# Performance work log

Measured on AMD Instinct MI355X. Metric: run time of the kernel, lower is better.

## Reference

```python
import jax, jax.numpy as jnp
import numpy as np

B, S, H = 2, 2048, 2048          # batch, seq, hidden_size
E, K = 16, 4                     # n_routed_experts, num_experts_per_tok
I = 1408                         # moe_intermediate_size
NS = 2                           # n_shared_experts
SI = I * NS                      # shared-expert intermediate size


def _mlp(x, wg, wu, wd):
    # SwiGLU MLP: down( silu(gate(x)) * up(x) )
    return (jax.nn.silu(x @ wg.T) * (x @ wu.T)) @ wd.T


def setup_inputs() -> dict:
    key = jax.random.key(0)
    ks = jax.random.split(key, 8)
    sc = lambda k, shape, fan: (jax.random.normal(k, shape, jnp.float32) * (fan ** -0.5))
    return {
        "hidden_states": jax.random.normal(ks[0], (B, S, H), jnp.float32),
        "gate_w": sc(ks[1], (E, H), H),          # router logits weight
        "w_gate": sc(ks[2], (E, I, H), H),       # per-expert gate_proj
        "w_up": sc(ks[3], (E, I, H), H),         # per-expert up_proj
        "w_down": sc(ks[4], (E, H, I), I),       # per-expert down_proj
        "sw_gate": sc(ks[5], (SI, H), H),        # shared-expert gate_proj
        "sw_up": sc(ks[6], (SI, H), H),
        "sw_down": sc(ks[7], (H, SI), SI),
    }


def reference(hidden_states, gate_w, w_gate, w_up, w_down, sw_gate, sw_up, sw_down):
    x = hidden_states.reshape(-1, H)                     # [T, H]
    T = x.shape[0]
    # --- MoEGate: softmax scoring, top-k, normalize weights to sum 1 ---
    scores = jax.nn.softmax(x @ gate_w.T, axis=-1)       # [T, E]
    topk_w, topk_idx = jax.lax.top_k(scores, K)          # [T, K]
    topk_w = topk_w / jnp.sum(topk_w, axis=-1, keepdims=True)
    # Dense combine weights [T, E]: cw[t, e] = sum_k 1[topk_idx==e] * topk_w
    cw = jnp.zeros((T, E), x.dtype).at[jnp.arange(T)[:, None], topk_idx].add(topk_w)
    # --- dispatch / per-expert MLP / weighted combine (scan over experts) ---
    def step(acc, p):
        wg, wu, wd, w = p                                # w: [T] combine weight
        return acc + w[:, None] * _mlp(x, wg, wu, wd), None
    y, _ = jax.lax.scan(step, jnp.zeros_like(x), (w_gate, w_up, w_down, cw.T))
    y = y.reshape(hidden_states.shape)
    # --- shared experts ---
    return y + _mlp(hidden_states, sw_gate, sw_up, sw_down)
```

## Files before the change

kernel.cpp:

```cpp
#include <hip/hip_runtime.h>
#include <cstdint>
#include <cstddef>

#define TTOK 4096
#define HID  2048
#define NEXP 16
#define KTOP 4
#define IMID 1408
#define SIM  2816

typedef __attribute__((ext_vector_type(4))) float f32x4;
typedef __attribute__((ext_vector_type(8))) short s16x8;
typedef __attribute__((ext_vector_type(4))) short s16x4;

#define OFF_XB   0UL
#define OFF_WGB  (OFF_XB  + 16777216UL)
#define OFF_WUB  (OFF_WGB + 92274688UL)
#define OFF_WDB  (OFF_WUB + 92274688UL)
#define OFF_SWG  (OFF_WDB + 92274688UL)
#define OFF_SWU  (OFF_SWG + 11534336UL)
#define OFF_SWD  (OFF_SWU + 11534336UL)
#define OFF_TKI  (OFF_SWD + 11534336UL)
#define OFF_TKW  (OFF_TKI + 65536UL)
#define OFF_CNT  (OFF_TKW + 65536UL)
#define OFF_OFFS (OFF_CNT + 64UL)
#define OFF_CUR  (OFF_OFFS + 64UL)
#define OFF_LIST (OFF_CUR + 64UL)
#define OFF_ACT  (OFF_LIST + 65536UL)
#define OFF_DOUT (OFF_ACT + 46137344UL)
#define OFF_SACT OFF_ACT

__device__ __forceinline__ unsigned short f2bf(float f) {
    unsigned int u = __float_as_uint(f);
    return (unsigned short)((u + 0x7FFFu + ((u >> 16) & 1u)) >> 16);
}
__device__ __forceinline__ float bf2f(unsigned short s) {
    return __uint_as_float(((unsigned int)s) << 16);
}
__device__ __forceinline__ void gll16(const void* g, void* l) {
    __builtin_amdgcn_global_load_lds((const __attribute__((address_space(1))) unsigned int*)g,
                                     (__attribute__((address_space(3))) unsigned int*)l, 16, 0, 0);
}

__global__ __launch_bounds__(256) void cast_k(const float* __restrict__ in,
                                              unsigned short* __restrict__ out, long n) {
    long i = ((long)blockIdx.x * 256 + threadIdx.x) * 4;
    if (i >= n) return;
    f32x4 v = *(const f32x4*)(in + i);
    s16x4 o;
    o.x = (short)f2bf(v.x); o.y = (short)f2bf(v.y);
    o.z = (short)f2bf(v.z); o.w = (short)f2bf(v.w);
    *(s16x4*)(out + i) = o;
}

__global__ __launch_bounds__(64) void route_k(const float* __restrict__ x,
                                              const float* __restrict__ gw,
                                              int* __restrict__ tki, float* __restrict__ tkw) {
    int t = blockIdx.x;
    int lane = threadIdx.x;
    const float* xr = x + (size_t)t * HID;
    float acc[NEXP];
#pragma unroll
    for (int e = 0; e < NEXP; e++) acc[e] = 0.f;
    for (int h = lane; h < HID; h += 64) {
        float xv = xr[h];
#pragma unroll
        for (int e = 0; e < NEXP; e++) acc[e] += xv * gw[e * HID + h];
    }
#pragma unroll
    for (int e = 0; e < NEXP; e++) {
        float v = acc[e];
#pragma unroll
        for (int off = 32; off; off >>= 1) v += __shfl_xor(v, off);
        acc[e] = v;
    }
    if (lane == 0) {
        float mx = acc[0];
#pragma unroll
        for (int e = 1; e < NEXP; e++) mx = fmaxf(mx, acc[e]);
        float s = 0.f, p[NEXP];
#pragma unroll
        for (int e = 0; e < NEXP; e++) { p[e] = expf(acc[e] - mx); s += p[e]; }
#pragma unroll
        for (int e = 0; e < NEXP; e++) p[e] /= s;
        float wsum = 0.f; int idx[KTOP]; float wv[KTOP];
#pragma unroll
        for (int k = 0; k < KTOP; k++) {
            int bi = 0; float bv = -1.f;
#pragma unroll
            for (int e = 0; e < NEXP; e++) if (p[e] > bv) { bv = p[e]; bi = e; }
            idx[k] = bi; wv[k] = bv; p[bi] = -2.f; wsum += bv;
        }
#pragma unroll
        for (int k = 0; k < KTOP; k++) { tki[t * 4 + k] = idx[k]; tkw[t * 4 + k] = wv[k] / wsum; }
    }
}

__global__ __launch_bounds__(256) void count_k(const int* __restrict__ tki, int* __restrict__ cnt) {
    int i = blockIdx.x * 256 + threadIdx.x;
    if (i < TTOK * KTOP) atomicAdd(&cnt[tki[i]], 1);
}
__global__ void scan_k(const int* __restrict__ cnt, int* __restrict__ offs, int* __restrict__ cur) {
    if (threadIdx.x == 0) {
        int s = 0;
        for (int e = 0; e < NEXP; e++) { offs[e] = s; cur[e] = s; s += cnt[e]; }
    }
}
__global__ __launch_bounds__(256) void scatter_k(const int* __restrict__ tki, int* __restrict__ cur,
                                                 int* __restrict__ list) {
    int i = blockIdx.x * 256 + threadIdx.x;
    if (i < TTOK * KTOP) {
        int e = tki[i];
        int p = atomicAdd(&cur[e], 1);
        list[p] = i;
    }
}

template <int MODE>
__global__ __launch_bounds__(256, 2) void gemm_k(const unsigned short* __restrict__ A,
                                                 const unsigned short* __restrict__ B0,
                                                 const unsigned short* __restrict__ B1,
                                                 void* __restrict__ C,
                                                 const int* __restrict__ counts,
                                                 const int* __restrict__ offs,
                                                 const int* __restrict__ list,
                                                 const float* __restrict__ tkw) {
    constexpr bool GU = (MODE == 0 || MODE == 1);
    constexpr bool ROUTED = (MODE == 0 || MODE == 2);
    constexpr int KD = (MODE == 2) ? IMID : ((MODE == 3) ? SIM : HID);
    constexpr int ND = (MODE == 0) ? IMID : ((MODE == 1) ? SIM : HID);
    constexpr int NB = ND / 128;

    int tid = threadIdx.x, lane = tid & 63, wv = tid >> 6;
    int bid = blockIdx.x;
    int e = 0, mb, nb, cnt, off;
    if (ROUTED) {
        e = bid / (32 * NB);
        int r = bid - e * (32 * NB);
        mb = r / NB; nb = r - mb * NB;
        cnt = counts[e]; off = offs[e];
        if (mb * 128 >= cnt) return;
    } else {
        mb = bid / NB; nb = bid - mb * NB; cnt = TTOK; off = 0;
    }

    const unsigned short* b0 = B0;
    const unsigned short* b1 = B1;
    if (MODE == 0) { b0 += (size_t)e * IMID * HID; b1 += (size_t)e * IMID * HID; }
    if (MODE == 2) { b0 += (size_t)e * HID * IMID; }

    const char* arow[2];
    const char* brow0[2];
    const char* brow1[2];
#pragma unroll
    for (int q = 0; q < 2; q++) {
        int r = mb * 128 + q * 64 + (tid >> 2);
        int rr = r < cnt ? r : cnt - 1;
        if (MODE == 0) { int tk = list[off + rr] >> 2; arow[q] = (const char*)(A + (size_t)tk * HID); }
        if (MODE == 1) { arow[q] = (const char*)(A + (size_t)rr * HID); }
        if (MODE == 2) { arow[q] = (const char*)(A + (size_t)(off + rr) * IMID); }
        if (MODE == 3) { arow[q] = (const char*)(A + (size_t)rr * SIM); }
        int rn = nb * 128 + q * 64 + (tid >> 2);
        brow0[q] = (const char*)(b0 + (size_t)rn * KD);
        if (GU) brow1[q] = (const char*)(b1 + (size_t)rn * KD);
    }

    constexpr int SBYTES = GU ? 24576 : 16384;
    __shared__ __align__(64) char smem[SBYTES];
    int inner = (lane & 3) * 16;
    char* ldsA  = smem + wv * 1024;
    char* ldsB0 = smem + 8192 + wv * 1024;
    char* ldsB1 = smem + 16384 + wv * 1024;

    f32x4 acc0[4][4], acc1[4][4];
#pragma unroll
    for (int i = 0; i < 4; i++)
#pragma unroll
        for (int j = 0; j < 4; j++) {
            acc0[i][j] = (f32x4){0.f, 0.f, 0.f, 0.f};
            acc1[i][j] = (f32x4){0.f, 0.f, 0.f, 0.f};
        }

    int wm = wv >> 1, wn = wv & 1;
    const unsigned short* rA  = (const unsigned short*)smem +
                                (wm * 64 + (lane & 15)) * 32 + ((lane >> 4) << 3);
    const unsigned short* rB0 = (const unsigned short*)(smem + 8192) +
                                (wn * 64 + (lane & 15)) * 32 + ((lane >> 4) << 3);
    const unsigned short* rB1 = (const unsigned short*)(smem + 16384) +
                                (wn * 64 + (lane & 15)) * 32 + ((lane >> 4) << 3);

    for (int k0 = 0; k0 < KD; k0 += 32) {
        size_t kb = (size_t)k0 * 2 + inner;
#pragma unroll
        for (int q = 0; q < 2; q++) {
            gll16(arow[q] + kb, ldsA + q * 4096);
            gll16(brow0[q] + kb, ldsB0 + q * 4096);
            if (GU) gll16(brow1[q] + kb, ldsB1 + q * 4096);
        }
        asm volatile("s_waitcnt vmcnt(0)" ::: "memory");
        __syncthreads();

        s16x8 af[4], bf0[4], bf1[4];
#pragma unroll
        for (int i = 0; i < 4; i++) {
            af[i] = *(const s16x8*)(rA + i * 16 * 32);
            bf0[i] = *(const s16x8*)(rB0 + i * 16 * 32);
            if (GU) bf1[i] = *(const s16x8*)(rB1 + i * 16 * 32);
        }
#pragma unroll
        for (int mi = 0; mi < 4; mi++)
#pragma unroll
            for (int ni = 0; ni < 4; ni++) {
                acc0[mi][ni] = __builtin_amdgcn_mfma_f32_16x16x32_bf16(af[mi], bf0[ni], acc0[mi][ni], 0, 0, 0);
                if (GU)
                    acc1[mi][ni] = __builtin_amdgcn_mfma_f32_16x16x32_bf16(af[mi], bf1[ni], acc1[mi][ni], 0, 0, 0);
            }
        __syncthreads();
    }

    int c0 = nb * 128 + wn * 64 + (lane & 15);
    int rb = mb * 128 + wm * 64 + ((lane >> 4) << 2);

    if (GU) {
        unsigned short* outp = (unsigned short*)C;
#pragma unroll
        for (int mi = 0; mi < 4; mi++)
#pragma unroll
            for (int j = 0; j < 4; j++) {
                int gr = rb + mi * 16 + j;
                if (gr < cnt) {
                    size_t orow = (size_t)(ROUTED ? (off + gr) : gr);
                    unsigned short* op = outp + orow * ND + c0;
#pragma unroll
                    for (int ni = 0; ni < 4; ni++) {
                        float g = acc0[mi][ni][j], u = acc1[mi][ni][j];
                        float v = (g / (1.f + expf(-g))) * u;
                        op[ni * 16] = f2bf(v);
                    }
                }
            }
    } else if (MODE == 2) {
        unsigned short* outp = (unsigned short*)C;
#pragma unroll
        for (int mi = 0; mi < 4; mi++)
#pragma unroll
            for (int j = 0; j < 4; j++) {
                int gr = rb + mi * 16 + j;
                if (gr < cnt) {
                    int en = list[off + gr];
                    float w = tkw[en];
                    unsigned short* op = outp + (size_t)en * HID + c0;
#pragma unroll
                    for (int ni = 0; ni < 4; ni++) op[ni * 16] = f2bf(acc0[mi][ni][j] * w);
                }
            }
    } else {
        float* outp = (float*)C;
#pragma unroll
        for (int mi = 0; mi < 4; mi++)
#pragma unroll
            for (int j = 0; j < 4; j++) {
                int gr = rb + mi * 16 + j;
                float* op = outp + (size_t)gr * HID + c0;
#pragma unroll
                for (int ni = 0; ni < 4; ni++) op[ni * 16] = acc0[mi][ni][j];
            }
    }
}

__global__ __launch_bounds__(256) void combine_k(const unsigned short* __restrict__ dout,
                                                 float* __restrict__ y) {
    long i = ((long)blockIdx.x * 256 + threadIdx.x) * 4;
    int t = (int)(i >> 11);
    int h = (int)(i & 2047);
    f32x4 acc = *(f32x4*)(y + i);
#pragma unroll
    for (int k = 0; k < 4; k++) {
        s16x4 dv = *(const s16x4*)(dout + (((size_t)t * 4 + k) << 11) + h);
        acc.x += bf2f((unsigned short)dv.x);
        acc.y += bf2f((unsigned short)dv.y);
        acc.z += bf2f((unsigned short)dv.z);
        acc.w += bf2f((unsigned short)dv.w);
    }
    *(f32x4*)(y + i) = acc;
}

extern "C" void kernel_launch(void* const* d_in, const int* in_sizes, int n_in,
                              void* d_out, int out_size, void* d_ws, size_t ws_size,
                              hipStream_t stream) {
    const float* x   = (const float*)d_in[0];
    const float* gw  = (const float*)d_in[1];
    const float* wg  = (const float*)d_in[2];
    const float* wu  = (const float*)d_in[3];
    const float* wd  = (const float*)d_in[4];
    const float* swg = (const float*)d_in[5];
    const float* swu = (const float*)d_in[6];
    const float* swd = (const float*)d_in[7];

    char* ws = (char*)d_ws;
    unsigned short* xb   = (unsigned short*)(ws + OFF_XB);
    unsigned short* wgb  = (unsigned short*)(ws + OFF_WGB);
    unsigned short* wub  = (unsigned short*)(ws + OFF_WUB);
    unsigned short* wdb  = (unsigned short*)(ws + OFF_WDB);
    unsigned short* swgb = (unsigned short*)(ws + OFF_SWG);
    unsigned short* swub = (unsigned short*)(ws + OFF_SWU);
    unsigned short* swdb = (unsigned short*)(ws + OFF_SWD);
    int*   tki  = (int*)(ws + OFF_TKI);
    float* tkw  = (float*)(ws + OFF_TKW);
    int*   cnt  = (int*)(ws + OFF_CNT);
    int*   offs = (int*)(ws + OFF_OFFS);
    int*   cur  = (int*)(ws + OFF_CUR);
    int*   list = (int*)(ws + OFF_LIST);
    unsigned short* act  = (unsigned short*)(ws + OFF_ACT);
    unsigned short* dout = (unsigned short*)(ws + OFF_DOUT);
    unsigned short* sact = (unsigned short*)(ws + OFF_SACT);
    float* y = (float*)d_out;

    hipMemsetAsync(ws + OFF_CNT, 0, 192, stream);

    auto cast = [&](const float* in, unsigned short* out, long n) {
        int blocks = (int)((n / 4 + 255) / 256);
        cast_k<<<blocks, 256, 0, stream>>>(in, out, n);
    };
    cast(x,   xb,   (long)TTOK * HID);
    cast(wg,  wgb,  (long)NEXP * IMID * HID);
    cast(wu,  wub,  (long)NEXP * IMID * HID);
    cast(wd,  wdb,  (long)NEXP * HID * IMID);
    cast(swg, swgb, (long)SIM * HID);
    cast(swu, swub, (long)SIM * HID);
    cast(swd, swdb, (long)HID * SIM);

    route_k<<<TTOK, 64, 0, stream>>>(x, gw, tki, tkw);
    count_k<<<TTOK * KTOP / 256, 256, 0, stream>>>(tki, cnt);
    scan_k<<<1, 64, 0, stream>>>(cnt, offs, cur);
    scatter_k<<<TTOK * KTOP / 256, 256, 0, stream>>>(tki, cur, list);

    gemm_k<0><<<NEXP * 32 * (IMID / 128), 256, 0, stream>>>(xb, wgb, wub, act, cnt, offs, list, tkw);
    gemm_k<2><<<NEXP * 32 * (HID / 128), 256, 0, stream>>>(act, wdb, nullptr, dout, cnt, offs, list, tkw);
    gemm_k<1><<<(TTOK / 128) * (SIM / 128), 256, 0, stream>>>(xb, swgb, swub, sact, cnt, offs, list, tkw);
    gemm_k<3><<<(TTOK / 128) * (HID / 128), 256, 0, stream>>>(sact, swdb, nullptr, (void*)y, cnt, offs, list, tkw);

    combine_k<<<TTOK * HID / 4 / 256, 256, 0, stream>>>(dout, y);
}
```

Baseline: 1.446 ms.

## Double-buffer GEMM LDS staging, swizzle block order, and widen cast vectors

The GEMM main loop now double-buffers LDS, issuing the next K-slice's global-to-LDS loads before computing on the current one. This removes the full wait-then-compute serialization of each iteration. It also adds an MFMA-friendly LDS layout where each lane reads a contiguous 16-byte chunk, a block-index remap that interleaves by 8 and walks M-tiles fastest, s_setprio around the MFMA block, and a launch_bounds occupancy hint of 3. The cast kernel now handles 8 elements per thread. Risks: LDS use doubles, which may limit occupancy, and the remaining vmcnt wait placement is implicit, so prefetched data may not be guaranteed complete before it is read.

```diff
diff --git a/kernel.cpp b/kernel.cpp
--- a/kernel.cpp
+++ b/kernel.cpp
@@ -44,13 +44,16 @@
 
 __global__ __launch_bounds__(256) void cast_k(const float* __restrict__ in,
                                               unsigned short* __restrict__ out, long n) {
-    long i = ((long)blockIdx.x * 256 + threadIdx.x) * 4;
+    long i = ((long)blockIdx.x * 256 + threadIdx.x) * 8;
     if (i >= n) return;
-    f32x4 v = *(const f32x4*)(in + i);
-    s16x4 o;
-    o.x = (short)f2bf(v.x); o.y = (short)f2bf(v.y);
-    o.z = (short)f2bf(v.z); o.w = (short)f2bf(v.w);
-    *(s16x4*)(out + i) = o;
+    f32x4 a = *(const f32x4*)(in + i);
+    f32x4 b = *(const f32x4*)(in + i + 4);
+    s16x8 o;
+    o[0] = (short)f2bf(a.x); o[1] = (short)f2bf(a.y);
+    o[2] = (short)f2bf(a.z); o[3] = (short)f2bf(a.w);
+    o[4] = (short)f2bf(b.x); o[5] = (short)f2bf(b.y);
+    o[6] = (short)f2bf(b.z); o[7] = (short)f2bf(b.w);
+    *(s16x8*)(out + i) = o;
 }
 
 __global__ __launch_bounds__(64) void route_k(const float* __restrict__ x,
@@ -117,7 +120,7 @@
 }
 
 template <int MODE>
-__global__ __launch_bounds__(256, 2) void gemm_k(const unsigned short* __restrict__ A,
+__global__ __launch_bounds__(256, 3) void gemm_k(const unsigned short* __restrict__ A,
                                                  const unsigned short* __restrict__ B0,
                                                  const unsigned short* __restrict__ B1,
                                                  void* __restrict__ C,
@@ -132,16 +135,19 @@
     constexpr int NB = ND / 128;
 
     int tid = threadIdx.x, lane = tid & 63, wv = tid >> 6;
-    int bid = blockIdx.x;
+
+    int nwg8 = (int)gridDim.x >> 3;
+    int bid = (blockIdx.x & 7) * nwg8 + (blockIdx.x >> 3);
+
     int e = 0, mb, nb, cnt, off;
     if (ROUTED) {
         e = bid / (32 * NB);
         int r = bid - e * (32 * NB);
-        mb = r / NB; nb = r - mb * NB;
+        nb = r >> 5; mb = r & 31;
         cnt = counts[e]; off = offs[e];
         if (mb * 128 >= cnt) return;
     } else {
-        mb = bid / NB; nb = bid - mb * NB; cnt = TTOK; off = 0;
+        nb = bid >> 5; mb = bid & 31; cnt = TTOK; off = 0;
     }
 
     const unsigned short* b0 = B0;
@@ -149,28 +155,40 @@
     if (MODE == 0) { b0 += (size_t)e * IMID * HID; b1 += (size_t)e * IMID * HID; }
     if (MODE == 2) { b0 += (size_t)e * HID * IMID; }
 
-    const char* arow[2];
-    const char* brow0[2];
-    const char* brow1[2];
+    const char* asrc[2];
+    const char* b0src[2];
+    const char* b1src[2];
 #pragma unroll
     for (int q = 0; q < 2; q++) {
-        int r = mb * 128 + q * 64 + (tid >> 2);
+        int st = 2 * wv + q;
+        int rt = st * 16 + (lane & 15);
+        int r = mb * 128 + rt;
         int rr = r < cnt ? r : cnt - 1;
-        if (MODE == 0) { int tk = list[off + rr] >> 2; arow[q] = (const char*)(A + (size_t)tk * HID); }
-        if (MODE == 1) { arow[q] = (const char*)(A + (size_t)rr * HID); }
-        if (MODE == 2) { arow[q] = (const char*)(A + (size_t)(off + rr) * IMID); }
-        if (MODE == 3) { arow[q] = (const char*)(A + (size_t)rr * SIM); }
-        int rn = nb * 128 + q * 64 + (tid >> 2);
-        brow0[q] = (const char*)(b0 + (size_t)rn * KD);
-        if (GU) brow1[q] = (const char*)(b1 + (size_t)rn * KD);
-    }
-
-    constexpr int SBYTES = GU ? 24576 : 16384;
-    __shared__ __align__(64) char smem[SBYTES];
-    int inner = (lane & 3) * 16;
-    char* ldsA  = smem + wv * 1024;
-    char* ldsB0 = smem + 8192 + wv * 1024;
-    char* ldsB1 = smem + 16384 + wv * 1024;
+        const unsigned short* ap;
+        if (MODE == 0) { int tk = list[off + rr] >> 2; ap = A + (size_t)tk * HID; }
+        else if (MODE == 1) { ap = A + (size_t)rr * HID; }
+        else if (MODE == 2) { ap = A + (size_t)(off + rr) * IMID; }
+        else { ap = A + (size_t)rr * SIM; }
+        asrc[q] = (const char*)ap + ((lane >> 4) << 4);
+        int rn = nb * 128 + rt;
+        b0src[q] = (const char*)(b0 + (size_t)rn * KD) + ((lane >> 4) << 4);
+        if (GU) b1src[q] = (const char*)(b1 + (size_t)rn * KD) + ((lane >> 4) << 4);
+    }
+
+    constexpr int BUFSZ = GU ? 24576 : 16384;
+    __shared__ __align__(1024) char smem[2 * BUFSZ];
+
+    auto stage = [&](int buf, int k0) {
+        char* base = smem + buf * BUFSZ;
+        size_t kb = (size_t)k0 * 2;
+#pragma unroll
+        for (int q = 0; q < 2; q++) {
+            int st = 2 * wv + q;
+            gll16(asrc[q] + kb, base + st * 1024);
+            gll16(b0src[q] + kb, base + 8192 + st * 1024);
+            if constexpr (GU) gll16(b1src[q] + kb, base + 16384 + st * 1024);
+        }
+    };
 
     f32x4 acc0[4][4], acc1[4][4];
 #pragma unroll
@@ -182,46 +200,44 @@
         }
 
     int wm = wv >> 1, wn = wv & 1;
-    const unsigned short* rA  = (const unsigned short*)smem +
-                                (wm * 64 + (lane & 15)) * 32 + ((lane >> 4) << 3);
-    const unsigned short* rB0 = (const unsigned short*)(smem + 8192) +
-                                (wn * 64 + (lane & 15)) * 32 + ((lane >> 4) << 3);
-    const unsigned short* rB1 = (const unsigned short*)(smem + 16384) +
-                                (wn * 64 + (lane & 15)) * 32 + ((lane >> 4) << 3);
-
+    int raoff = (wm * 4) * 1024 + lane * 16;
+    int rboff = 8192 + (wn * 4) * 1024 + lane * 16;
+    int rb1off = 16384 + (wn * 4) * 1024 + lane * 16;
+
+    stage(0, 0);
+    asm volatile("s_waitcnt vmcnt(0)" ::: "memory");
+    __syncthreads();
+
+    int cur = 0;
     for (int k0 = 0; k0 < KD; k0 += 32) {
-        size_t kb = (size_t)k0 * 2 + inner;
-#pragma unroll
-        for (int q = 0; q < 2; q++) {
-            gll16(arow[q] + kb, ldsA + q * 4096);
-            gll16(brow0[q] + kb, ldsB0 + q * 4096);
-            if (GU) gll16(brow1[q] + kb, ldsB1 + q * 4096);
+        if (k0 + 32 < KD) stage(cur ^ 1, k0 + 32);
+
+        const char* bufp = smem + cur * BUFSZ;
+        s16x8 af[4], bv0[4], bv1[4];
+#pragma unroll
+        for (int i = 0; i < 4; i++) {
+            af[i]  = *(const s16x8*)(bufp + raoff + i * 1024);
+            bv0[i] = *(const s16x8*)(bufp + rboff + i * 1024);
+            if constexpr (GU) bv1[i] = *(const s16x8*)(bufp + rb1off + i * 1024);
         }
-        asm volatile("s_waitcnt vmcnt(0)" ::: "memory");
+        __builtin_amdgcn_s_setprio(1);
+#pragma unroll
+        for (int mi = 0; mi < 4; mi++)
+#pragma unroll
+            for (int ni = 0; ni < 4; ni++) {
+                acc0[mi][ni] = __builtin_amdgcn_mfma_f32_16x16x32_bf16(af[mi], bv0[ni], acc0[mi][ni], 0, 0, 0);
+                if constexpr (GU)
+                    acc1[mi][ni] = __builtin_amdgcn_mfma_f32_16x16x32_bf16(af[mi], bv1[ni], acc1[mi][ni], 0, 0, 0);
+            }
+        __builtin_amdgcn_s_setprio(0);
         __syncthreads();
-
-        s16x8 af[4], bf0[4], bf1[4];
-#pragma unroll
-        for (int i = 0; i < 4; i++) {
-            af[i] = *(const s16x8*)(rA + i * 16 * 32);
-            bf0[i] = *(const s16x8*)(rB0 + i * 16 * 32);
-            if (GU) bf1[i] = *(const s16x8*)(rB1 + i * 16 * 32);
-        }
-#pragma unroll
-        for (int mi = 0; mi < 4; mi++)
-#pragma unroll
-            for (int ni = 0; ni < 4; ni++) {
-                acc0[mi][ni] = __builtin_amdgcn_mfma_f32_16x16x32_bf16(af[mi], bf0[ni], acc0[mi][ni], 0, 0, 0);
-                if (GU)
-                    acc1[mi][ni] = __builtin_amdgcn_mfma_f32_16x16x32_bf16(af[mi], bf1[ni], acc1[mi][ni], 0, 0, 0);
-            }
-        __syncthreads();
+        cur ^= 1;
     }
 
     int c0 = nb * 128 + wn * 64 + (lane & 15);
     int rb = mb * 128 + wm * 64 + ((lane >> 4) << 2);
 
-    if (GU) {
+    if constexpr (GU) {
         unsigned short* outp = (unsigned short*)C;
 #pragma unroll
         for (int mi = 0; mi < 4; mi++)
@@ -239,7 +255,7 @@
                     }
                 }
             }
-    } else if (MODE == 2) {
+    } else if constexpr (MODE == 2) {
         unsigned short* outp = (unsigned short*)C;
 #pragma unroll
         for (int mi = 0; mi < 4; mi++)
@@ -319,7 +335,7 @@
     hipMemsetAsync(ws + OFF_CNT, 0, 192, stream);
 
     auto cast = [&](const float* in, unsigned short* out, long n) {
-        int blocks = (int)((n / 4 + 255) / 256);
+        int blocks = (int)((n / 8 + 255) / 256);
         cast_k<<<blocks, 256, 0, stream>>>(in, out, n);
     };
     cast(x,   xb,   (long)TTOK * HID);
```

Result: slower. 2.682 ms (+85.5%).
